# Performance work log

Hardware: AMD Instinct MI355X
Metric: run time of the kernel (lower is better)

Reference implementation:

```python
import math
import jax, jax.numpy as jnp
import numpy as np

N_LAYERS = 2
D = 256        # d_input
N = 32         # d_state
BATCH = 8
L = 2048
SPK = 2


def setup_inputs() -> dict:
    key = jax.random.key(0)
    ks = jax.random.split(key, 20)
    def rn(i, shape, s=1.0):
        return jax.random.normal(ks[i], shape, jnp.float32) * s
    w = 0.02  # weight init scale
    lo, hi = math.log(1e-3), math.log(1e-1)
    return dict(
        x=rn(0, (BATCH, D, L)),
        ln_g=jnp.ones((N_LAYERS, 2, D), jnp.float32),
        ln_b=jnp.zeros((N_LAYERS, 2, D), jnp.float32),
        log_dt=lo + jax.random.uniform(ks[1], (N_LAYERS, D), jnp.float32) * (hi - lo),
        A_log_re=rn(2, (N_LAYERS, D, N), 0.5),
        A_im=rn(3, (N_LAYERS, D, N)) * math.pi,
        B_re=rn(4, (N_LAYERS, D, N), 0.5),
        B_im=rn(5, (N_LAYERS, D, N), 0.5),
        C_re=rn(6, (N_LAYERS, D, N), 0.5),
        C_im=rn(7, (N_LAYERS, D, N), 0.5),
        Dp=rn(8, (N_LAYERS, D)),
        s4o_W=rn(9, (N_LAYERS, D, D), w), s4o_b=jnp.zeros((N_LAYERS, D), jnp.float32),
        lin1_W=rn(10, (N_LAYERS, D, D), w), lin1_b=jnp.zeros((N_LAYERS, D), jnp.float32),
        lin2_W=rn(11, (N_LAYERS, D, D), w), lin2_b=jnp.zeros((N_LAYERS, D), jnp.float32),
        out_W0=rn(12, (D, D), w), out_b0=jnp.zeros((D,), jnp.float32),
        proj_W0=rn(13, (D, D), w), proj_b0=jnp.zeros((D,), jnp.float32),
        out_W1=rn(14, (D, SPK * D), w), out_b1=jnp.zeros((SPK * D,), jnp.float32),
        proj_W1=rn(15, (D, SPK * D), w), proj_b1=jnp.zeros((SPK * D,), jnp.float32),
    )


def _layernorm(x, g, b, eps=1e-5):
    m = jnp.mean(x, axis=-1, keepdims=True)
    v = jnp.var(x, axis=-1, keepdims=True)
    return (x - m) * jax.lax.rsqrt(v + eps) * g + b


def _s4(u, log_dt, A_log_re, A_im, B_re, B_im, C_re, C_im, Dp, oW, ob):
    # u: [B, L, H]. Diagonal SSM (ZOH discretization) -> global FFT convolution.
    Lq = u.shape[1]
    dt = jnp.exp(log_dt)                       # [H]
    A = -jnp.exp(A_log_re) + 1j * A_im         # [H, N], Re(A) < 0 for stability
    dtA = dt[:, None] * A                      # [H, N]
    dB = (B_re + 1j * B_im) * (jnp.exp(dtA) - 1.0) / A
    CB = (C_re + 1j * C_im) * dB               # [H, N]
    steps = jnp.arange(Lq)
    # Vandermonde kernel K[h, l] = 2 Re sum_n CB[h,n] * exp(dtA[h,n] * l)
    K = 2.0 * jnp.einsum('hn,hnl->hl', CB, jnp.exp(dtA[:, :, None] * steps)).real
    n = 2 * Lq  # linear (non-circular) convolution
    Uf = jnp.fft.rfft(u, n=n, axis=1)          # [B, nf, H]
    Kf = jnp.fft.rfft(K, n=n, axis=-1)         # [H, nf]
    y = jnp.fft.irfft(Uf * Kf.T[None], n=n, axis=1)[:, :Lq]
    y = y + u * Dp                              # skip connection D*u
    y = jax.nn.gelu(y, approximate=False)       # S4 activation='gelu'
    return y @ oW + ob                          # output_linear (postact='id')


def reference(x, ln_g, ln_b, log_dt, A_log_re, A_im, B_re, B_im, C_re, C_im, Dp,
              s4o_W, s4o_b, lin1_W, lin1_b, lin2_W, lin2_b,
              out_W0, out_b0, proj_W0, proj_b0, out_W1, out_b1, proj_W1, proj_b1):
    o = jnp.moveaxis(x, -1, -2)  # [B, L, D]
    heads = [(out_W0, out_b0, proj_W0, proj_b0), (out_W1, out_b1, proj_W1, proj_b1)]
    for i in range(N_LAYERS):
        oW, ob, pW, pb = heads[i]
        u = o
        o1 = _layernorm(u, ln_g[i, 0], ln_b[i, 0])
        o1 = _s4(o1, log_dt[i], A_log_re[i], A_im[i], B_re[i], B_im[i],
                 C_re[i], C_im[i], Dp[i], s4o_W[i], s4o_b[i])
        o1 = o1 @ lin1_W[i] + lin1_b[i] + u     # residual add
        o2 = _layernorm(o1, ln_g[i, 1], ln_b[i, 1])
        o2 = jax.nn.gelu(o2 @ lin2_W[i] + lin2_b[i], approximate=False)
        o = o2 @ oW + ob + (o1 @ pW + pb)
    o = jax.nn.relu(o)                          # output_activation
    Bsz, Lq, C = o.shape
    d = C // SPK
    o = jnp.moveaxis(o, -1, 0).reshape(SPK, d, Bsz, Lq)
    return jnp.moveaxis(o, 1, -2)               # [num_spks, B, d_input, L]
```

## Files before the change

kernel.cpp:

```cpp
#include <hip/hip_runtime.h>


#define BSZ 8
#define DM 256
#define LSEQ 2048
#define NST 32
#define TC 64
#define NCH 32
#define TOK (BSZ*LSEQ)
#define NL 2

typedef __attribute__((ext_vector_type(8))) short bf16x8;
typedef __attribute__((ext_vector_type(4))) float f32x4;
typedef unsigned short ushort_t;

__device__ __forceinline__ float b2f(unsigned short v) {
    unsigned int u = ((unsigned int)v) << 16;
    float f;
    __builtin_memcpy(&f, &u, 4);
    return f;
}
__device__ __forceinline__ unsigned short f2b(float f) {
    unsigned int u;
    __builtin_memcpy(&u, &f, 4);
    unsigned int r = (u + 0x7FFFu + ((u >> 16) & 1u)) >> 16;
    return (unsigned short)r;
}
__device__ __forceinline__ float gelu_f(float z) {
    float x = z * 0.70710678118654752f;
    float ax = fabsf(x);
    float t = 1.0f / (1.0f + 0.3275911f * ax);
    float poly = t * (0.254829592f + t * (-0.284496736f + t * (1.421413741f +
                 t * (-1.453152027f + t * 1.061405429f))));
    float erfax = 1.0f - poly * expf(-ax * ax);
    float er = (x < 0.0f) ? -erfax : erfax;
    return 0.5f * z * (1.0f + er);
}

__global__ void k_setup_modes(const float* log_dt, const float* Alr, const float* Aim,
                              const float* Bre, const float* Bim,
                              const float* Cre, const float* Cim,
                              float2* dtA, float2* lam, float2* lamT, float2* CB) {
    int idx = blockIdx.x * blockDim.x + threadIdx.x;
    if (idx >= NL * DM * NST) return;
    int h = (idx >> 5) & (DM - 1);
    int i = idx >> 13;
    float dt  = expf(log_dt[i * DM + h]);
    float Are = -expf(Alr[idx]);
    float Ai  = Aim[idx];
    float dr = dt * Are, di = dt * Ai;
    float er = expf(dr);
    float lr = er * cosf(di), li = er * sinf(di);
    float inv = 1.0f / (Are * Are + Ai * Ai);
    float e1r = lr - 1.0f, e1i = li;
    float tr = (e1r * Are + e1i * Ai) * inv;
    float ti = (e1i * Are - e1r * Ai) * inv;
    float br = Bre[idx], bi = Bim[idx];
    float dBr = br * tr - bi * ti, dBi = br * ti + bi * tr;
    float cr = Cre[idx], ci = Cim[idx];
    dtA[idx] = make_float2(dr, di);
    lam[idx] = make_float2(lr, li);
    CB[idx]  = make_float2(cr * dBr - ci * dBi, cr * dBi + ci * dBr);
    float pr = lr, pi = li;
    for (int s = 0; s < 6; ++s) { float nr = pr * pr - pi * pi; pi = 2.f * pr * pi; pr = nr; }
    lamT[idx] = make_float2(pr, pi);
}

__global__ void k_wcvt(const float* src, ushort_t* dst, int N) {
    int idx = blockIdx.x * 256 + threadIdx.x;
    if (idx >= N * 256) return;
    int n = idx >> 8, k = idx & 255;
    dst[idx] = f2b(src[(size_t)k * N + n]);
}

__global__ void k_wc_fuse(const float* Wa, const float* Wb, ushort_t* WBc) {
    int c = blockIdx.x;
    int r = threadIdx.x;
    const float* ar = Wa + (size_t)r * 256;
    float s = 0.f;
    for (int k = 0; k < 256; ++k) s = fmaf(ar[k], Wb[(size_t)k * 256 + c], s);
    WBc[(size_t)c * 256 + r] = f2b(s);
}
__global__ void k_bc_fuse(const float* s4ob, const float* Wb, const float* lin1b,
                          float* bc) {
    int c = threadIdx.x;
    float s = lin1b[c];
    for (int k = 0; k < 256; ++k) s = fmaf(s4ob[k], Wb[(size_t)k * 256 + c], s);
    bc[c] = s;
}

__global__ void k_setup_wk(const float2* dtA_l, const float2* lam_l, const float2* CB_l,
                           float* Ktab, float2* Wtab) {
    int idx = blockIdx.x * blockDim.x + threadIdx.x;
    if (idx >= DM * TC) return;
    int t = idx & (TC - 1);
    int h = idx >> 6;
    int base = h * NST;
    float ft = (float)t;
    float Ks = 0.f;
    for (int n = 0; n < NST; ++n) {
        float2 d = dtA_l[base + n]; float2 l1 = lam_l[base + n]; float2 cb = CB_l[base + n];
        float er = expf(d.x * ft);
        float cs = cosf(d.y * ft), sn = sinf(d.y * ft);
        float ltr = er * cs, lti = er * sn;
        Ks += cb.x * ltr - cb.y * lti;
        float p1r = ltr * l1.x - lti * l1.y, p1i = ltr * l1.y + lti * l1.x;
        Wtab[(h * NST + n) * TC + t] =
            make_float2(cb.x * p1r - cb.y * p1i, cb.x * p1i + cb.y * p1r);
    }
    Ktab[idx] = 2.f * Ks;
}

__global__ void k_transpose_in(const float* x, ushort_t* o) {
    __shared__ float tile[32][33];
    int b = blockIdx.z;
    int l0 = blockIdx.x * 32, d0 = blockIdx.y * 32;
    int tx = threadIdx.x, ty = threadIdx.y;
    for (int k = 0; k < 4; ++k)
        tile[ty + 8 * k][tx] = x[((size_t)b * DM + d0 + ty + 8 * k) * LSEQ + l0 + tx];
    __syncthreads();
    for (int k = 0; k < 4; ++k)
        o[((size_t)b * LSEQ + l0 + ty + 8 * k) * DM + d0 + tx] = f2b(tile[tx][ty + 8 * k]);
}

__global__ void k_layernorm(const ushort_t* src, ushort_t* dst,
                            const float* g, const float* bb) {
    __shared__ float r1[DM];
    __shared__ float r2[DM];
    int tok = blockIdx.x;
    int d = threadIdx.x;
    float v = b2f(src[(size_t)tok * DM + d]);
    r1[d] = v;
    r2[d] = v * v;
    __syncthreads();
    for (int s = DM / 2; s > 0; s >>= 1) {
        if (d < s) { r1[d] += r1[d + s]; r2[d] += r2[d + s]; }
        __syncthreads();
    }
    float m = r1[0] * (1.0f / DM);
    float var = r2[0] * (1.0f / DM) - m * m;
    float inv = rsqrtf(var + 1e-5f);
    dst[(size_t)tok * DM + d] = f2b((v - m) * inv * g[d] + bb[d]);
}

__global__ void k_layernorm_T(const ushort_t* src, ushort_t* dstT,
                              const float* g, const float* bb) {
    __shared__ float r1[DM];
    __shared__ float r2[DM];
    int tok = blockIdx.x;
    int d = threadIdx.x;
    float v = b2f(src[(size_t)tok * DM + d]);
    r1[d] = v;
    r2[d] = v * v;
    __syncthreads();
    for (int s = DM / 2; s > 0; s >>= 1) {
        if (d < s) { r1[d] += r1[d + s]; r2[d] += r2[d + s]; }
        __syncthreads();
    }
    float m = r1[0] * (1.0f / DM);
    float var = r2[0] * (1.0f / DM) - m * m;
    float inv = rsqrtf(var + 1e-5f);
    int b = tok >> 11, l = tok & 2047;
    dstT[((size_t)b * DM + d) * LSEQ + l] = f2b((v - m) * inv * g[d] + bb[d]);
}

__global__ void k_chunk_states(const ushort_t* uT, const float2* lam_l, float2* P) {
    int n = threadIdx.x & 31, hs = threadIdx.x >> 5;
    int c = blockIdx.x, h = blockIdx.y * 8 + hs, b = blockIdx.z;
    float2 lm = lam_l[h * NST + n];
    float sr = 0.f, si = 0.f;
    const ushort_t* up = uT + ((size_t)b * DM + h) * LSEQ + c * TC;
#pragma unroll 8
    for (int t = 0; t < TC; ++t) {
        float u = b2f(up[t]);
        float nr = fmaf(lm.x, sr, fmaf(-lm.y, si, u));
        float ni = fmaf(lm.x, si, lm.y * sr);
        sr = nr; si = ni;
    }
    P[(((size_t)b * DM + h) * NCH + c) * NST + n] = make_float2(sr, si);
}

__global__ void k_chunk_scan(const float2* lamT_l, float2* P) {
    int idx = blockIdx.x * blockDim.x + threadIdx.x;
    if (idx >= BSZ * DM * NST) return;
    int n = idx & 31, h = (idx >> 5) & 255, b = idx >> 13;
    float2 lT = lamT_l[h * NST + n];
    float hr = 0.f, hi = 0.f;
    float2* base = P + (((size_t)b * DM + h) * NCH) * NST + n;
    for (int c = 0; c < NCH; ++c) {
        float2 p = base[(size_t)c * NST];
        base[(size_t)c * NST] = make_float2(hr, hi);
        float nr = fmaf(lT.x, hr, fmaf(-lT.y, hi, p.x));
        float ni = fmaf(lT.x, hi, fmaf(lT.y, hr, p.y));
        hr = nr; hi = ni;
    }
}

__global__ void k_conv_mfma(const ushort_t* uT, ushort_t* G, const float* Ktab,
                            const float2* Wtab, const float2* P, const float* Dp_l) {
    __shared__ ushort_t As[64][128];
    __shared__ ushort_t Bs[256][128];
    int h = blockIdx.x;
    int tid = threadIdx.x;
    int wv = tid >> 6, l = tid & 63;
    for (int idx = tid; idx < 64 * 128; idx += 256) {
        int r = idx >> 7, e = idx & 127;
        float v;
        if (e < 64) {
            int d = r - e;
            v = (d >= 0) ? Ktab[h * TC + d] : 0.f;
        } else {
            int j = e - 64;
            float2 wc = Wtab[((size_t)h * NST + (j >> 1)) * TC + r];
            v = (j & 1) ? -2.f * wc.y : 2.f * wc.x;
        }
        As[r][e ^ ((r & 7) << 3)] = f2b(v);
    }
    for (int idx = tid; idx < 256 * 8; idx += 256) {
        int row = idx >> 3, ch = (idx & 7) * 8;
        int b = row >> 5, c = row & 31;
        bf16x8 v = *(const bf16x8*)(uT + ((size_t)b * DM + h) * LSEQ + c * TC + ch);
        *(bf16x8*)(&Bs[row][ch ^ ((row & 7) << 3)]) = v;
    }
    for (int idx = tid; idx < 256 * 32; idx += 256) {
        int row = idx >> 5, n = idx & 31;
        int b = row >> 5, c = row & 31;
        float2 s = P[(((size_t)b * DM + h) * NCH + c) * NST + n];
        int x = (row & 7) << 3;
        Bs[row][(64 + 2 * n) ^ x]     = f2b(s.x);
        Bs[row][(64 + 2 * n + 1) ^ x] = f2b(s.y);
    }
    __syncthreads();
    int lr = l & 15, lk = (l >> 4) * 8;
    int ax = (lr & 7) << 3;
    f32x4 acc[16];
#pragma unroll
    for (int i = 0; i < 16; ++i) acc[i] = (f32x4){0.f, 0.f, 0.f, 0.f};
#pragma unroll
    for (int k0 = 0; k0 < 128; k0 += 32) {
        bf16x8 a = *(const bf16x8*)(&As[wv * 16 + lr][(lk + k0) ^ ax]);
#pragma unroll
        for (int nt = 0; nt < 16; ++nt) {
            bf16x8 b = *(const bf16x8*)(&Bs[nt * 16 + lr][(lk + k0) ^ ax]);
            acc[nt] = __builtin_amdgcn_mfma_f32_16x16x32_bf16(a, b, acc[nt], 0, 0, 0);
        }
    }
    float dp = Dp_l[h];
#pragma unroll
    for (int nt = 0; nt < 16; ++nt) {
        int bc = nt * 16 + (l & 15);
        int b = bc >> 5, c = bc & 31;
        int bx = (bc & 7) << 3;
#pragma unroll
        for (int r = 0; r < 4; ++r) {
            int t = wv * 16 + (l >> 4) * 4 + r;
            float uv = b2f(Bs[bc][t ^ bx]);
            float z = acc[nt][r] + dp * uv;
            G[((size_t)b * LSEQ + c * TC + t) * DM + h] = f2b(gelu_f(z));
        }
    }
}

__device__ __forceinline__ void stage_tile(const ushort_t* src, int row0,
                                           ushort_t (*dst)[256], int tid) {
    for (int idx = tid; idx < 64 * 32; idx += 256) {
        int r = idx >> 5, ch = (idx & 31) * 8;
        bf16x8 v = *(const bf16x8*)(src + (size_t)(row0 + r) * 256 + ch);
        *(bf16x8*)(&dst[r][ch ^ ((r & 7) << 3)]) = v;
    }
}
__device__ __forceinline__ void mma_tile(const ushort_t (*As)[256],
                                         const ushort_t (*Bs)[256],
                                         int wv, int l, f32x4* acc) {
    int lr = l & 15, lk = (l >> 4) * 8;
    int ax = (lr & 7) << 3;
#pragma unroll
    for (int k0 = 0; k0 < 256; k0 += 32) {
        bf16x8 a  = *(const bf16x8*)(&As[wv * 16 + lr][(lk + k0) ^ ax]);
        bf16x8 b0 = *(const bf16x8*)(&Bs[lr]          [(lk + k0) ^ ax]);
        bf16x8 b1 = *(const bf16x8*)(&Bs[16 + lr]     [(lk + k0) ^ ax]);
        bf16x8 b2 = *(const bf16x8*)(&Bs[32 + lr]     [(lk + k0) ^ ax]);
        bf16x8 b3 = *(const bf16x8*)(&Bs[48 + lr]     [(lk + k0) ^ ax]);
        acc[0] = __builtin_amdgcn_mfma_f32_16x16x32_bf16(a, b0, acc[0], 0, 0, 0);
        acc[1] = __builtin_amdgcn_mfma_f32_16x16x32_bf16(a, b1, acc[1], 0, 0, 0);
        acc[2] = __builtin_amdgcn_mfma_f32_16x16x32_bf16(a, b2, acc[2], 0, 0, 0);
        acc[3] = __builtin_amdgcn_mfma_f32_16x16x32_bf16(a, b3, acc[3], 0, 0, 0);
    }
}

__global__ void k_gemm_mfma(const ushort_t* A, const ushort_t* WBt,
                            const float* bias, const ushort_t* res,
                            ushort_t* C, int N, int flags) {
    __shared__ ushort_t As[64][256];
    __shared__ ushort_t Bs[64][256];
    int m0 = blockIdx.x * 64, n0 = blockIdx.y * 64;
    int tid = threadIdx.x;
    int wv = tid >> 6, l = tid & 63;
    stage_tile(A, m0, As, tid);
    stage_tile(WBt, n0, Bs, tid);
    __syncthreads();
    f32x4 acc[4] = {{0,0,0,0},{0,0,0,0},{0,0,0,0},{0,0,0,0}};
    mma_tile(As, Bs, wv, l, acc);
    int em = m0 + wv * 16 + (l >> 4) * 4;
    int en = n0 + (l & 15);
#pragma unroll
    for (int nt = 0; nt < 4; ++nt) {
        int n = en + nt * 16;
        float bsv = bias[n];
#pragma unroll
        for (int r = 0; r < 4; ++r) {
            int m = em + r;
            float v = acc[nt][r] + bsv;
            if (res) v += b2f(res[(size_t)m * DM + n]);
            if (flags & 1) v = gelu_f(v);
            if (flags & 8) v = fmaxf(v, 0.0f);
            C[(size_t)m * N + n] = f2b(v);
        }
    }
}

__global__ void k_gemm2_mfma(const ushort_t* Aa, const ushort_t* WBa,
                             const ushort_t* Ab, const ushort_t* WBb,
                             const float* biasA, const float* biasB,
                             ushort_t* C, int N, int flags) {
    __shared__ ushort_t As[64][256];
    __shared__ ushort_t Bs[64][256];
    int m0 = blockIdx.x * 64, n0 = blockIdx.y * 64;
    int tid = threadIdx.x;
    int wv = tid >> 6, l = tid & 63;
    f32x4 acc[4] = {{0,0,0,0},{0,0,0,0},{0,0,0,0},{0,0,0,0}};
    stage_tile(Aa, m0, As, tid);
    stage_tile(WBa, n0, Bs, tid);
    __syncthreads();
    mma_tile(As, Bs, wv, l, acc);
    __syncthreads();
    stage_tile(Ab, m0, As, tid);
    stage_tile(WBb, n0, Bs, tid);
    __syncthreads();
    mma_tile(As, Bs, wv, l, acc);
    int em = m0 + wv * 16 + (l >> 4) * 4;
    int en = n0 + (l & 15);
#pragma unroll
    for (int nt = 0; nt < 4; ++nt) {
        int n = en + nt * 16;
        float bsv = biasA[n] + biasB[n];
#pragma unroll
        for (int r = 0; r < 4; ++r) {
            int m = em + r;
            float v = acc[nt][r] + bsv;
            if (flags & 8) v = fmaxf(v, 0.0f);
            C[(size_t)m * N + n] = f2b(v);
        }
    }
}

__global__ void k_final_out(const ushort_t* F, float* out) {
    __shared__ float tile[32][33];
    int b = blockIdx.z;
    int l0 = blockIdx.x * 32, c0 = blockIdx.y * 32;
    int tx = threadIdx.x, ty = threadIdx.y;
    for (int k = 0; k < 4; ++k)
        tile[ty + 8 * k][tx] = b2f(F[((size_t)(b * LSEQ + l0 + ty + 8 * k)) * 512 + c0 + tx]);
    __syncthreads();
    for (int k = 0; k < 4; ++k) {
        int cg = c0 + ty + 8 * k;
        int s = cg >> 8, cc = cg & 255;
        out[(((size_t)s * BSZ + b) * DM + cc) * LSEQ + l0 + tx] = tile[tx][ty + 8 * k];
    }
}

extern "C" void kernel_launch(void* const* d_in, const int* in_sizes, int n_in,
                              void* d_out, int out_size, void* d_ws, size_t ws_size,
                              hipStream_t stream) {
    (void)in_sizes; (void)n_in; (void)out_size;
    float* out = (float*)d_out;

    const float* x      = (const float*)d_in[0];
    const float* ln_g   = (const float*)d_in[1];
    const float* ln_b   = (const float*)d_in[2];
    const float* log_dt = (const float*)d_in[3];
    const float* Alr    = (const float*)d_in[4];
    const float* Aim    = (const float*)d_in[5];
    const float* Bre    = (const float*)d_in[6];
    const float* Bim    = (const float*)d_in[7];
    const float* Cre    = (const float*)d_in[8];
    const float* Cim    = (const float*)d_in[9];
    const float* Dp     = (const float*)d_in[10];
    const float* s4oW   = (const float*)d_in[11];
    const float* s4ob   = (const float*)d_in[12];
    const float* lin1W  = (const float*)d_in[13];
    const float* lin1b  = (const float*)d_in[14];
    const float* lin2W  = (const float*)d_in[15];
    const float* lin2b  = (const float*)d_in[16];
    const float* headW[2] = {(const float*)d_in[17], (const float*)d_in[21]};
    const float* headb[2] = {(const float*)d_in[18], (const float*)d_in[22]};
    const float* projW[2] = {(const float*)d_in[19], (const float*)d_in[23]};
    const float* projb[2] = {(const float*)d_in[20], (const float*)d_in[24]};

    char* w = (char*)d_ws;
    ushort_t* A0 = (ushort_t*)w;  w += (size_t)TOK * DM * 2;
    ushort_t* A1 = (ushort_t*)w;  w += (size_t)TOK * DM * 2;
    ushort_t* A2 = (ushort_t*)w;  w += (size_t)TOK * DM * 2;
    float2* dtA  = (float2*)w;    w += (size_t)NL * DM * NST * 8;
    float2* lam  = (float2*)w;    w += (size_t)NL * DM * NST * 8;
    float2* lamT = (float2*)w;    w += (size_t)NL * DM * NST * 8;
    float2* CB   = (float2*)w;    w += (size_t)NL * DM * NST * 8;
    float2* P    = (float2*)w;    w += (size_t)BSZ * DM * NCH * NST * 8;
    float2* Wtab = (float2*)w;    w += (size_t)DM * NST * TC * 8;
    float*  KtabC = (float*)w;    w += (size_t)DM * TC * 4;
    ushort_t* wb = (ushort_t*)w;  w += (size_t)655360 * 2;
    float*  bc   = (float*)w;     w += 512 * 4;
    if ((size_t)(w - (char*)d_ws) > ws_size) return;
    ushort_t* F = (ushort_t*)P;

    ushort_t* WB_lin2[2] = {wb + 0,      wb + 65536};
    ushort_t* WB_head0   = wb + 131072;
    ushort_t* WB_proj0   = wb + 196608;
    ushort_t* WB_head1   = wb + 262144;
    ushort_t* WB_proj1   = wb + 393216;
    ushort_t* WBc[2]     = {wb + 524288, wb + 589824};

    k_setup_modes<<<NL * DM * NST / 256, 256, 0, stream>>>(
        log_dt, Alr, Aim, Bre, Bim, Cre, Cim, dtA, lam, lamT, CB);
    for (int i = 0; i < NL; ++i) {
        size_t wf = (size_t)i * DM * DM;
        k_wcvt<<<256, 256, 0, stream>>>(lin2W + wf, WB_lin2[i], DM);
        k_wc_fuse<<<256, 256, 0, stream>>>(s4oW + wf, lin1W + wf, WBc[i]);
        k_bc_fuse<<<1, 256, 0, stream>>>(s4ob + i * DM, lin1W + wf, lin1b + i * DM,
                                         bc + i * 256);
    }
    k_wcvt<<<256, 256, 0, stream>>>(headW[0], WB_head0, DM);
    k_wcvt<<<256, 256, 0, stream>>>(projW[0], WB_proj0, DM);
    k_wcvt<<<512, 256, 0, stream>>>(headW[1], WB_head1, 2 * DM);
    k_wcvt<<<512, 256, 0, stream>>>(projW[1], WB_proj1, 2 * DM);
    {
        dim3 gt(LSEQ / 32, DM / 32, BSZ);
        dim3 bt(32, 8);
        k_transpose_in<<<gt, bt, 0, stream>>>(x, A0);
    }

    dim3 gg(TOK / 64, DM / 64);
    for (int i = 0; i < NL; ++i) {
        ushort_t* U = (i == 0) ? A0 : A2;
        ushort_t* T = (i == 0) ? A1 : A0;
        ushort_t* G = (i == 0) ? A2 : A1;
        size_t off = (size_t)i * DM * NST;

        k_layernorm_T<<<TOK, DM, 0, stream>>>(U, T, ln_g + (2 * i) * DM,
                                              ln_b + (2 * i) * DM);
        k_setup_wk<<<DM * TC / 128, 128, 0, stream>>>(dtA + off, lam + off,
                                                      CB + off, KtabC, Wtab);
        {
            dim3 gs(NCH, DM / 8, BSZ);
            k_chunk_states<<<gs, 256, 0, stream>>>(T, lam + off, P);
        }
        k_chunk_scan<<<BSZ * DM * NST / 256, 256, 0, stream>>>(lamT + off, P);
        k_conv_mfma<<<DM, 256, 0, stream>>>(T, G, KtabC, Wtab, P, Dp + i * DM);
        k_gemm_mfma<<<gg, 256, 0, stream>>>(G, WBc[i], bc + i * 256, U, T, DM, 0);
        k_layernorm<<<TOK, DM, 0, stream>>>(T, G, ln_g + (2 * i + 1) * DM,
                                            ln_b + (2 * i + 1) * DM);
        k_gemm_mfma<<<gg, 256, 0, stream>>>(G, WB_lin2[i], lin2b + i * DM, 0, U, DM, 1);
        if (i == 0) {
            k_gemm2_mfma<<<gg, 256, 0, stream>>>(U, WB_head0, T, WB_proj0,
                                                 headb[0], projb[0], A2, DM, 0);
        } else {
            dim3 gh(TOK / 64, 2 * DM / 64);
            k_gemm2_mfma<<<gh, 256, 0, stream>>>(U, WB_head1, T, WB_proj1,
                                                 headb[1], projb[1], F, 2 * DM, 8);
        }
    }
    {
        dim3 gf(LSEQ / 32, 2 * DM / 32, BSZ);
        dim3 bf(32, 8);
        k_final_out<<<gf, bf, 0, stream>>>(F, out);
    }
}
```

Measured before the change: 458.0 us.

## Remap GEMM blocks per XCD and stage epilogue through LDS for vector stores

The GEMM kernels now remap the flat block index so that consecutive blocks landing on the same XCD cover contiguous M tiles across all N tiles, aiming to improve L2 reuse of the A rows. The epilogue first writes the accumulators into shared memory, then each thread reads back a contiguous 16-element row segment, applies bias, residual and activation, and writes two 16-byte bf16 vectors. This replaces scattered 2-byte global stores with coalesced vector stores, at the cost of an extra LDS round trip and two more barriers. The mapping assumes gridDim.x is a multiple of 8.

```diff
diff --git a/kernel.cpp b/kernel.cpp
--- a/kernel.cpp
+++ b/kernel.cpp
@@ -287,13 +287,34 @@
         acc[3] = __builtin_amdgcn_mfma_f32_16x16x32_bf16(a, b3, acc[3], 0, 0, 0);
     }
 }
+__device__ __forceinline__ void xcd_map(int* m0, int* n0) {
+    int flat = blockIdx.y * gridDim.x + blockIdx.x;
+    int xcd = flat & 7;
+    int wl = flat >> 3;
+    int nt = gridDim.y;
+    int n_t = wl % nt;
+    int m_t = xcd * (gridDim.x >> 3) + wl / nt;
+    *m0 = m_t * 64;
+    *n0 = n_t * 64;
+}
+#define OTP 66
+__device__ __forceinline__ void epi_store(float* Ot, int wv, int l, f32x4* acc) {
+    int lrow = wv * 16 + (l >> 4) * 4;
+    int lcol = l & 15;
+#pragma unroll
+    for (int nt = 0; nt < 4; ++nt)
+#pragma unroll
+        for (int r = 0; r < 4; ++r)
+            Ot[(lrow + r) * OTP + lcol + nt * 16] = acc[nt][r];
+}
 
 __global__ void k_gemm_mfma(const ushort_t* A, const ushort_t* WBt,
                             const float* bias, const ushort_t* res,
                             ushort_t* C, int N, int flags) {
     __shared__ ushort_t As[64][256];
     __shared__ ushort_t Bs[64][256];
-    int m0 = blockIdx.x * 64, n0 = blockIdx.y * 64;
+    int m0, n0;
+    xcd_map(&m0, &n0);
     int tid = threadIdx.x;
     int wv = tid >> 6, l = tid & 63;
     stage_tile(A, m0, As, tid);
@@ -301,22 +322,23 @@
     __syncthreads();
     f32x4 acc[4] = {{0,0,0,0},{0,0,0,0},{0,0,0,0},{0,0,0,0}};
     mma_tile(As, Bs, wv, l, acc);
-    int em = m0 + wv * 16 + (l >> 4) * 4;
-    int en = n0 + (l & 15);
-#pragma unroll
-    for (int nt = 0; nt < 4; ++nt) {
-        int n = en + nt * 16;
-        float bsv = bias[n];
-#pragma unroll
-        for (int r = 0; r < 4; ++r) {
-            int m = em + r;
-            float v = acc[nt][r] + bsv;
-            if (res) v += b2f(res[(size_t)m * DM + n]);
-            if (flags & 1) v = gelu_f(v);
-            if (flags & 8) v = fmaxf(v, 0.0f);
-            C[(size_t)m * N + n] = f2b(v);
-        }
-    }
+    __syncthreads();
+    float* Ot = (float*)As;
+    epi_store(Ot, wv, l, acc);
+    __syncthreads();
+    int row = tid >> 2, cs = (tid & 3) * 16;
+    int m = m0 + row;
+    ushort_t ov[16];
+#pragma unroll
+    for (int j = 0; j < 16; ++j) {
+        float v = Ot[row * OTP + cs + j] + bias[n0 + cs + j];
+        if (res) v += b2f(res[(size_t)m * DM + n0 + cs + j]);
+        if (flags & 1) v = gelu_f(v);
+        if (flags & 8) v = fmaxf(v, 0.0f);
+        ov[j] = f2b(v);
+    }
+    *(bf16x8*)(C + (size_t)m * N + n0 + cs)     = *(bf16x8*)(ov);
+    *(bf16x8*)(C + (size_t)m * N + n0 + cs + 8) = *(bf16x8*)(ov + 8);
 }
 
 __global__ void k_gemm2_mfma(const ushort_t* Aa, const ushort_t* WBa,
@@ -325,7 +347,8 @@
                              ushort_t* C, int N, int flags) {
     __shared__ ushort_t As[64][256];
     __shared__ ushort_t Bs[64][256];
-    int m0 = blockIdx.x * 64, n0 = blockIdx.y * 64;
+    int m0, n0;
+    xcd_map(&m0, &n0);
     int tid = threadIdx.x;
     int wv = tid >> 6, l = tid & 63;
     f32x4 acc[4] = {{0,0,0,0},{0,0,0,0},{0,0,0,0},{0,0,0,0}};
@@ -338,20 +361,21 @@
     stage_tile(WBb, n0, Bs, tid);
     __syncthreads();
     mma_tile(As, Bs, wv, l, acc);
-    int em = m0 + wv * 16 + (l >> 4) * 4;
-    int en = n0 + (l & 15);
-#pragma unroll
-    for (int nt = 0; nt < 4; ++nt) {
-        int n = en + nt * 16;
-        float bsv = biasA[n] + biasB[n];
-#pragma unroll
-        for (int r = 0; r < 4; ++r) {
-            int m = em + r;
-            float v = acc[nt][r] + bsv;
-            if (flags & 8) v = fmaxf(v, 0.0f);
-            C[(size_t)m * N + n] = f2b(v);
-        }
-    }
+    __syncthreads();
+    float* Ot = (float*)As;
+    epi_store(Ot, wv, l, acc);
+    __syncthreads();
+    int row = tid >> 2, cs = (tid & 3) * 16;
+    int m = m0 + row;
+    ushort_t ov[16];
+#pragma unroll
+    for (int j = 0; j < 16; ++j) {
+        float v = Ot[row * OTP + cs + j] + biasA[n0 + cs + j] + biasB[n0 + cs + j];
+        if (flags & 8) v = fmaxf(v, 0.0f);
+        ov[j] = f2b(v);
+    }
+    *(bf16x8*)(C + (size_t)m * N + n0 + cs)     = *(bf16x8*)(ov);
+    *(bf16x8*)(C + (size_t)m * N + n0 + cs + 8) = *(bf16x8*)(ov + 8);
 }
 
 __global__ void k_final_out(const ushort_t* F, float* out) {
```

Result: slower. 470.7 us (median of 3 runs) (+2.8%).
